# Optimization experiments

Hardware: AMD Instinct MI355X
Metric: run time of the kernel (lower is better)

Reference implementation:

```python
import jax, jax.numpy as jnp
import numpy as np

HID, INNER, CONV, L, DR = 1024, 2048, 4, 16, 64
B, S = 1, 2048


def setup_inputs() -> dict:
    key = jax.random.key(0)
    ks = jax.random.split(key, 8)
    def n(k, shape, scale=0.02):
        return jax.random.normal(k, shape, jnp.float32) * scale
    x = jax.random.normal(ks[0], (B, S, HID), jnp.float32)
    W_in = n(ks[1], (HID, 2 * INNER))                 # input_proj kernel (no bias)
    conv_w = n(ks[2], (CONV, 1, INNER), 0.1)          # depthwise conv kernel (W, I/g, O)
    conv_b = n(ks[3], (INNER,), 0.01)                 # conv bias
    W_x = n(ks[4], (INNER, DR + 2 * L))               # x_proj kernel (no bias)
    W_delta = n(ks[5], (DR, INNER), 0.05)             # delta_proj kernel
    b_delta = jnp.zeros((INNER,), jnp.float32)        # delta_proj bias
    A_log = jnp.log(jnp.tile(jnp.arange(1, L + 1, dtype=jnp.float32), (INNER, 1)))
    D = jnp.ones((INNER,), jnp.float32)
    W_out = n(ks[6], (INNER, HID))                    # out_proj kernel (no bias)
    return dict(x=x, W_in=W_in, conv_w=conv_w, conv_b=conv_b, W_x=W_x,
                W_delta=W_delta, b_delta=b_delta, A_log=A_log, D=D, W_out=W_out)


def _combine(left, right):
    # Associative op for linear recurrence h_t = a_t * h_{t-1} + b_t
    a1, b1 = left
    a2, b2 = right
    return a1 * a2, a2 * b1 + b2


def reference(x, W_in, conv_w, conv_b, W_x, W_delta, b_delta, A_log, D, W_out):
    b, s, _ = x.shape
    xz = x @ W_in                                     # [b,s,2*INNER]
    xi, z = xz[..., :INNER], xz[..., INNER:]
    # depthwise causal-ish conv: pad conv_dim-1 both sides (flax int padding), keep first s
    xc = jax.lax.conv_general_dilated(
        xi, conv_w, window_strides=(1,), padding=[(CONV - 1, CONV - 1)],
        dimension_numbers=('NWC', 'WIO', 'NWC'), feature_group_count=INNER)
    xc = jax.nn.silu(xc[:, :s, :] + conv_b)           # [b,s,INNER]
    # selective SSM
    A = -jnp.exp(A_log.astype(jnp.float32))           # [INNER,L]
    Df = D.astype(jnp.float32)
    xp = xc @ W_x                                     # [b,s,DR+2L]
    delta, Bm, Cm = xp[..., :DR], xp[..., DR:DR + L], xp[..., DR + L:]
    delta = jax.nn.softplus(delta @ W_delta + b_delta)  # [b,s,INNER]
    deltaA = jnp.exp(jnp.einsum('bsd,dl->bsdl', delta, A))            # [b,s,d,l]
    deltaBx = jnp.einsum('bsd,bsl,bsd->bsdl', delta, Bm, xc)          # [b,s,d,l]
    _, h = jax.lax.associative_scan(_combine, (deltaA, deltaBx), axis=1)
    y = jnp.einsum('bsdl,bsl->bsd', h, Cm) + xc * Df  # [b,s,INNER]
    y = y * jax.nn.silu(z)
    return y @ W_out                                  # [b,s,HID]
```

## Files before the change

kernel.cpp:

```cpp
#include <hip/hip_runtime.h>
#include <hip/hip_bf16.h>
#include <math.h>

#define S_LEN 2048
#define HID   1024
#define INNER 2048
#define NCONV 4
#define LSTATE 16
#define DRANK 64
#define XPW   96
#define CHUNK 32
#define NCHUNK (S_LEN / CHUNK)
#define XPAD  128
#define XPSPLIT 16
#define OSPLIT  4

typedef __attribute__((ext_vector_type(8))) short bf16x8;
typedef __attribute__((ext_vector_type(4))) float f32x4;

__device__ __forceinline__ short f2bf(float f) {
  union { __hip_bfloat16 h; short s; } u;
  u.h = __float2bfloat16(f);
  return u.s;
}

__device__ __forceinline__ float fexp(float x) { return __expf(x); }

#define GLDS(gp, lp) __builtin_amdgcn_global_load_lds(                         \
    (const __attribute__((address_space(1))) unsigned int*)(gp),               \
    (__attribute__((address_space(3))) unsigned int*)(lp), 16, 0, 0)

#define NB_CAST (S_LEN * HID / 4 / 256)
#define NB_WIN  ((2 * INNER / 32) * (HID / 32))
#define NB_WOUT ((HID / 32) * (INNER / 32))
#define NB_WX   ((XPAD / 32) * (INNER / 32))
#define NB_WD   ((INNER / 32) * (DRANK / 32))
#define NB_PREP (NB_CAST + NB_WIN + NB_WOUT + NB_WX + NB_WD)
__global__ __launch_bounds__(256) void prep_kernel(
    const float* __restrict__ x, short* __restrict__ xb,
    const float* __restrict__ W_in, short* __restrict__ WinT,
    const float* __restrict__ W_out, short* __restrict__ WoutT,
    const float* __restrict__ W_x, short* __restrict__ WxT,
    const float* __restrict__ W_delta, short* __restrict__ WdT) {
  const int b = blockIdx.x;
  if (b < NB_CAST) {
    int i = b * 256 + threadIdx.x;
    const float4 v = ((const float4*)x)[i];
    short4 o;
    o.x = f2bf(v.x); o.y = f2bf(v.y); o.z = f2bf(v.z); o.w = f2bf(v.w);
    ((short4*)xb)[i] = o;
    return;
  }
  __shared__ float tile[32][33];
  const float* in; short* outp; int R, C, bx, by;
  if (b < NB_CAST + NB_WIN) {
    int bb = b - NB_CAST;
    in = W_in; outp = WinT; R = HID; C = 2 * INNER;
    bx = bb % (2 * INNER / 32); by = bb / (2 * INNER / 32);
  } else if (b < NB_CAST + NB_WIN + NB_WOUT) {
    int bb = b - NB_CAST - NB_WIN;
    in = W_out; outp = WoutT; R = INNER; C = HID;
    bx = bb % (HID / 32); by = bb / (HID / 32);
  } else if (b < NB_CAST + NB_WIN + NB_WOUT + NB_WX) {
    int bb = b - NB_CAST - NB_WIN - NB_WOUT;
    in = W_x; outp = WxT; R = INNER; C = XPW;
    bx = bb % (XPAD / 32); by = bb / (XPAD / 32);
  } else {
    int bb = b - NB_CAST - NB_WIN - NB_WOUT - NB_WX;
    in = W_delta; outp = WdT; R = DRANK; C = INNER;
    bx = bb % (INNER / 32); by = bb / (INNER / 32);
  }
  const int bc = bx * 32, br = by * 32;
  const int tx = threadIdx.x & 31, ty = threadIdx.x >> 5;
  #pragma unroll
  for (int i = 0; i < 32; i += 8)
    tile[ty + i][tx] = (bc + tx < C)
        ? in[(size_t)(br + ty + i) * C + bc + tx] : 0.f;
  __syncthreads();
  #pragma unroll
  for (int i = 0; i < 32; i += 8)
    outp[(size_t)(bc + ty + i) * R + br + tx] = f2bf(tile[tx][ty + i]);
}

#define BK   32
#define NBUF 4
template<int EPI>
__global__ __launch_bounds__(512) void gemm_bf16(
    const short* __restrict__ A,  int lda,
    const short* __restrict__ Bt, int ldb,
    float* __restrict__ C, int ldc,
    int kPerSplit, size_t cSliceStride,
    const float* __restrict__ bias) {
  __shared__ short As[NBUF][128 * BK];
  __shared__ short Bs[NBUF][128 * BK];
  const int tid  = threadIdx.x;
  const int lane = tid & 63;
  const int wave = tid >> 6;
  const int bm = blockIdx.y * 128;
  const int bn = blockIdx.x * 128;
  const int wm = (wave & 1) * 64;
  const int wn = (wave >> 1) * 32;
  const int fr = lane & 15;
  const int fq = lane >> 4;
  const int kbeg = blockIdx.z * kPerSplit;
  const int nIter = kPerSplit / BK;
  float* Cw = C + (size_t)blockIdx.z * cSliceStride;

  const int sw  = wave & 3;
  const int rs0 = sw * 32 + (lane >> 2);
  const int rs1 = rs0 + 16;
  const int sg0 = (lane & 3) ^ ((rs0 >> 1) & 3);
  const int sg1 = (lane & 3) ^ ((rs1 >> 1) & 3);
  const bool isB = wave >= 4;
  const short* gbase = isB ? Bt : A;
  const int    gld   = isB ? ldb : lda;
  const int    gro   = isB ? bn  : bm;
  const short* g0 = gbase + (size_t)(gro + rs0) * gld + kbeg + sg0 * 8;
  const short* g1 = gbase + (size_t)(gro + rs1) * gld + kbeg + sg1 * 8;
  const int lo0 = (sw * 32) * BK;
  const int lo1 = (sw * 32 + 16) * BK;

  f32x4 acc[4][2] = {};

#define STAGE(tile, buf) do {                                                  \
    short* dst_ = isB ? &Bs[buf][0] : &As[buf][0];                             \
    const int ko_ = (tile) * BK;                                               \
    GLDS(g0 + ko_, dst_ + lo0);                                                \
    GLDS(g1 + ko_, dst_ + lo1);                                                \
  } while (0)

  STAGE(0, 0);
  if (nIter > 1) STAGE(1, 1);
  if (nIter > 2) STAGE(2, 2);

  const int sl = (fq ^ ((fr >> 1) & 3)) * 8;
  for (int t = 0; t < nIter; ++t) {
    const int rem = nIter - 1 - t;
    if (rem >= 2)      asm volatile("s_waitcnt vmcnt(4)" ::: "memory");
    else if (rem == 1) asm volatile("s_waitcnt vmcnt(2)" ::: "memory");
    else               asm volatile("s_waitcnt vmcnt(0)" ::: "memory");
    asm volatile("s_barrier" ::: "memory");
    if (t + 3 < nIter) STAGE(t + 3, (t + 3) & 3);
    const int r = t & 3;
    bf16x8 af[4], bfv[2];
    #pragma unroll
    for (int mi = 0; mi < 4; ++mi)
      af[mi] = *(const bf16x8*)(&As[r][(wm + mi * 16 + fr) * BK + sl]);
    #pragma unroll
    for (int ni = 0; ni < 2; ++ni)
      bfv[ni] = *(const bf16x8*)(&Bs[r][(wn + ni * 16 + fr) * BK + sl]);
    #pragma unroll
    for (int mi = 0; mi < 4; ++mi)
      #pragma unroll
      for (int ni = 0; ni < 2; ++ni)
        acc[mi][ni] = __builtin_amdgcn_mfma_f32_16x16x32_bf16(
            af[mi], bfv[ni], acc[mi][ni], 0, 0, 0);
  }
#undef STAGE
  #pragma unroll
  for (int mi = 0; mi < 4; ++mi) {
    #pragma unroll
    for (int ni = 0; ni < 2; ++ni) {
      const int col = bn + wn + ni * 16 + fr;
      #pragma unroll
      for (int r = 0; r < 4; ++r) {
        const int row = bm + wm + mi * 16 + fq * 4 + r;
        float v = acc[mi][ni][r];
        if (EPI == 1) {
          v += bias[col];
          v = fmaxf(v, 0.f) + log1pf(expf(-fabsf(v)));
        }
        Cw[(size_t)row * ldc + col] = v;
      }
    }
  }
}

__global__ __launch_bounds__(256) void reduce_xp_kernel(
    const float* __restrict__ part, float* __restrict__ xp,
    short* __restrict__ xpb64) {
  int i4 = blockIdx.x * 256 + threadIdx.x;
  if (i4 >= S_LEN * (XPW / 4)) return;
  int m = i4 / (XPW / 4);
  int n4 = i4 - m * (XPW / 4);
  const float4* p = (const float4*)part;
  const size_t rowv = (size_t)m * (XPAD / 4) + n4;
  const size_t slice = (size_t)S_LEN * (XPAD / 4);
  float4 o = p[rowv];
  #pragma unroll
  for (int s = 1; s < XPSPLIT; ++s) {
    float4 v = p[rowv + s * slice];
    o.x += v.x; o.y += v.y; o.z += v.z; o.w += v.w;
  }
  ((float4*)xp)[i4] = o;
  if (n4 < DRANK / 4) {
    short4 s4;
    s4.x = f2bf(o.x); s4.y = f2bf(o.y); s4.z = f2bf(o.z); s4.w = f2bf(o.w);
    ((short4*)xpb64)[m * (DRANK / 4) + n4] = s4;
  }
}

__global__ __launch_bounds__(256) void reduce_out_kernel(
    const float* __restrict__ part, float* __restrict__ out) {
  int i4 = blockIdx.x * 256 + threadIdx.x;
  if (i4 >= S_LEN * (HID / 4)) return;
  const float4* p = (const float4*)part;
  const size_t slice = (size_t)S_LEN * (HID / 4);
  float4 o = p[i4];
  #pragma unroll
  for (int s = 1; s < OSPLIT; ++s) {
    float4 v = p[i4 + s * slice];
    o.x += v.x; o.y += v.y; o.z += v.z; o.w += v.w;
  }
  ((float4*)out)[i4] = o;
}

__global__ __launch_bounds__(256) void conv_silu_kernel(
    const float* __restrict__ xz,
    const float* __restrict__ cw,
    const float* __restrict__ cb,
    float* __restrict__ xc,
    short* __restrict__ xcb) {
  int i4 = blockIdx.x * 256 + threadIdx.x;
  if (i4 >= S_LEN * INNER / 4) return;
  int s = i4 / (INNER / 4);
  int cg = i4 - s * (INNER / 4);
  float4 acc = ((const float4*)cb)[cg];
  #pragma unroll
  for (int k = 0; k < NCONV; ++k) {
    int t = s - (NCONV - 1) + k;
    if (t >= 0) {
      float4 xv = *(const float4*)(xz + (size_t)t * (2 * INNER) + cg * 4);
      float4 wv = ((const float4*)(cw + k * INNER))[cg];
      acc.x += xv.x * wv.x; acc.y += xv.y * wv.y;
      acc.z += xv.z * wv.z; acc.w += xv.w * wv.w;
    }
  }
  float4 v;
  v.x = acc.x / (1.f + fexp(-acc.x));
  v.y = acc.y / (1.f + fexp(-acc.y));
  v.z = acc.z / (1.f + fexp(-acc.z));
  v.w = acc.w / (1.f + fexp(-acc.w));
  ((float4*)xc)[i4] = v;
  short4 o;
  o.x = f2bf(v.x); o.y = f2bf(v.y); o.z = f2bf(v.z); o.w = f2bf(v.w);
  ((short4*)xcb)[i4] = o;
}


__global__ __launch_bounds__(256) void scan_pass1(
    const float* __restrict__ delta,
    const float* __restrict__ xp,
    const float* __restrict__ xc,
    const float* __restrict__ A_log,
    float* __restrict__ Aprod,
    float* __restrict__ Hend) {
  __shared__ float Bc[CHUNK][LSTATE];
  const int tid = threadIdx.x;
  const int d = blockIdx.y * 256 + tid;
  const int c = blockIdx.x;
  const int s0 = c * CHUNK;
  for (int u = tid; u < CHUNK * LSTATE; u += 256) {
    int r = u >> 4, l = u & 15;
    Bc[r][l] = xp[(size_t)(s0 + r) * XPW + DRANK + l];
  }
  float a[LSTATE];
  {
    const float4* Ar = (const float4*)(A_log + (size_t)d * LSTATE);
    #pragma unroll
    for (int q = 0; q < 4; ++q) {
      float4 v = Ar[q];
      a[q * 4 + 0] = -fexp(v.x);
      a[q * 4 + 1] = -fexp(v.y);
      a[q * 4 + 2] = -fexp(v.z);
      a[q * 4 + 3] = -fexp(v.w);
    }
  }
  float h[LSTATE] = {}, ap[LSTATE];
  #pragma unroll
  for (int l = 0; l < LSTATE; ++l) ap[l] = 1.f;
  __syncthreads();
  const float* pd = delta + (size_t)s0 * INNER + d;
  const float* px = xc    + (size_t)s0 * INNER + d;
  for (int i = 0; i < CHUNK; ++i) {
    float dv = *pd, xcv = *px;
    pd += INNER; px += INNER;
    float sc = dv * xcv;
    #pragma unroll
    for (int l = 0; l < LSTATE; ++l) {
      float dA = fexp(dv * a[l]);
      h[l] = fmaf(dA, h[l], sc * Bc[i][l]);
      ap[l] *= dA;
    }
  }
  float4* Ap = (float4*)(Aprod + ((size_t)c * INNER + d) * LSTATE);
  float4* Hp = (float4*)(Hend  + ((size_t)c * INNER + d) * LSTATE);
  #pragma unroll
  for (int q = 0; q < 4; ++q) {
    Ap[q] = make_float4(ap[q * 4], ap[q * 4 + 1], ap[q * 4 + 2], ap[q * 4 + 3]);
    Hp[q] = make_float4(h[q * 4], h[q * 4 + 1], h[q * 4 + 2], h[q * 4 + 3]);
  }
}

__global__ __launch_bounds__(256) void scan_pass2(
    const float* __restrict__ Aprod, const float* __restrict__ Hend,
    float* __restrict__ Hin) {
  const int idx = blockIdx.x * 256 + threadIdx.x;
  const size_t stride = (size_t)INNER * LSTATE;
  float h = 0.f;
  for (int cb = 0; cb < NCHUNK; cb += 16) {
    float ap[16], he[16];
    #pragma unroll
    for (int j = 0; j < 16; ++j) {
      size_t o = (size_t)(cb + j) * stride + idx;
      ap[j] = Aprod[o];
      he[j] = Hend[o];
    }
    #pragma unroll
    for (int j = 0; j < 16; ++j) {
      size_t o = (size_t)(cb + j) * stride + idx;
      Hin[o] = h;
      h = ap[j] * h + he[j];
    }
  }
}

__global__ __launch_bounds__(256) void scan_pass3(
    const float* __restrict__ delta,
    const float* __restrict__ xp,
    const float* __restrict__ xc,
    const float* __restrict__ xz,
    const float* __restrict__ A_log,
    const float* __restrict__ Dvec,
    const float* __restrict__ Hin,
    short* __restrict__ ybf) {
  __shared__ float Bc[CHUNK][LSTATE];
  __shared__ float Cc[CHUNK][LSTATE];
  const int tid = threadIdx.x;
  const int d = blockIdx.y * 256 + tid;
  const int c = blockIdx.x;
  const int s0 = c * CHUNK;
  for (int u = tid; u < CHUNK * LSTATE; u += 256) {
    int r = u >> 4, l = u & 15;
    size_t base = (size_t)(s0 + r) * XPW + DRANK;
    Bc[r][l] = xp[base + l];
    Cc[r][l] = xp[base + LSTATE + l];
  }
  float a[LSTATE], h[LSTATE];
  {
    const float4* Ar = (const float4*)(A_log + (size_t)d * LSTATE);
    #pragma unroll
    for (int q = 0; q < 4; ++q) {
      float4 v = Ar[q];
      a[q * 4 + 0] = -fexp(v.x);
      a[q * 4 + 1] = -fexp(v.y);
      a[q * 4 + 2] = -fexp(v.z);
      a[q * 4 + 3] = -fexp(v.w);
    }
    const float4* Hi = (const float4*)(Hin + ((size_t)c * INNER + d) * LSTATE);
    #pragma unroll
    for (int q = 0; q < 4; ++q) {
      float4 v = Hi[q];
      h[q * 4 + 0] = v.x; h[q * 4 + 1] = v.y;
      h[q * 4 + 2] = v.z; h[q * 4 + 3] = v.w;
    }
  }
  const float Dd = Dvec[d];
  __syncthreads();
  const float* pd = delta + (size_t)s0 * INNER + d;
  const float* px = xc    + (size_t)s0 * INNER + d;
  const float* pz = xz + (size_t)s0 * (2 * INNER) + INNER + d;
  short* py = ybf + (size_t)s0 * INNER + d;
  for (int i = 0; i < CHUNK; ++i) {
    float dv = *pd, xcv = *px, zv = *pz;
    pd += INNER; px += INNER; pz += 2 * INNER;
    float sc = dv * xcv;
    float contrib = 0.f;
    #pragma unroll
    for (int l = 0; l < LSTATE; ++l) {
      float dA = fexp(dv * a[l]);
      h[l] = fmaf(dA, h[l], sc * Bc[i][l]);
      contrib = fmaf(h[l], Cc[i][l], contrib);
    }
    float silu_z = zv / (1.f + fexp(-zv));
    *py = f2bf(fmaf(xcv, Dd, contrib) * silu_z);
    py += INNER;
  }
}

extern "C" void kernel_launch(void* const* d_in, const int* in_sizes, int n_in,
                              void* d_out, int out_size, void* d_ws, size_t ws_size,
                              hipStream_t stream) {
  const float* x      = (const float*)d_in[0];
  const float* W_in   = (const float*)d_in[1];
  const float* conv_w = (const float*)d_in[2];
  const float* conv_b = (const float*)d_in[3];
  const float* W_x    = (const float*)d_in[4];
  const float* W_delta= (const float*)d_in[5];
  const float* b_delta= (const float*)d_in[6];
  const float* A_log  = (const float*)d_in[7];
  const float* Dvec   = (const float*)d_in[8];
  const float* W_out  = (const float*)d_in[9];
  float* out = (float*)d_out;

  float* ws    = (float*)d_ws;
  float* xz    = ws;
  float* xc    = xz + (size_t)S_LEN * 2 * INNER;
  float* xp    = xc + (size_t)S_LEN * INNER;
  float* delta = xp + (size_t)S_LEN * XPW;
  float* Aprod = delta + (size_t)S_LEN * INNER;
  float* Hend  = Aprod + (size_t)NCHUNK * INNER * LSTATE;
  float* Hin   = Hend  + (size_t)NCHUNK * INNER * LSTATE;
  short* xb    = (short*)(Hin + (size_t)NCHUNK * INNER * LSTATE);
  short* WinT  = xb + (size_t)S_LEN * HID;
  short* WoutT = WinT + (size_t)(2 * INNER) * HID;
  short* ybf   = WoutT + (size_t)HID * INNER;
  short* xcb   = ybf + (size_t)S_LEN * INNER;
  short* WxT   = xcb + (size_t)S_LEN * INNER;
  short* WdT   = WxT + (size_t)XPAD * INNER;
  short* xpb64 = WdT + (size_t)INNER * DRANK;
  float* xpPart  = Aprod;
  float* outPart = xc;

  prep_kernel<<<NB_PREP, 256, 0, stream>>>(
      x, xb, W_in, WinT, W_out, WoutT, W_x, WxT, W_delta, WdT);

  gemm_bf16<0><<<dim3(4096 / 128, 2048 / 128, 1), 512, 0, stream>>>(
      xb, HID, WinT, HID, xz, 2 * INNER, HID, 0, nullptr);

  conv_silu_kernel<<<(S_LEN * INNER / 4 + 255) / 256, 256, 0, stream>>>(
      xz, conv_w, conv_b, xc, xcb);

  gemm_bf16<0><<<dim3(1, 2048 / 128, XPSPLIT), 512, 0, stream>>>(
      xcb, INNER, WxT, INNER, xpPart, XPAD, INNER / XPSPLIT,
      (size_t)S_LEN * XPAD, nullptr);
  reduce_xp_kernel<<<(S_LEN * (XPW / 4) + 255) / 256, 256, 0, stream>>>(
      xpPart, xp, xpb64);

  gemm_bf16<1><<<dim3(2048 / 128, 2048 / 128, 1), 512, 0, stream>>>(
      xpb64, DRANK, WdT, DRANK, delta, INNER, DRANK, 0, b_delta);

  scan_pass1<<<dim3(NCHUNK, INNER / 256), 256, 0, stream>>>(
      delta, xp, xc, A_log, Aprod, Hend);
  scan_pass2<<<(INNER * LSTATE) / 256, 256, 0, stream>>>(Aprod, Hend, Hin);
  scan_pass3<<<dim3(NCHUNK, INNER / 256), 256, 0, stream>>>(
      delta, xp, xc, xz, A_log, Dvec, Hin, ybf);

  gemm_bf16<0><<<dim3(1024 / 128, 2048 / 128, OSPLIT), 512, 0, stream>>>(
      ybf, INNER, WoutT, INNER, outPart, HID, INNER / OSPLIT,
      (size_t)S_LEN * HID, nullptr);
  reduce_out_kernel<<<(S_LEN * (HID / 4) + 255) / 256, 256, 0, stream>>>(
      outPart, out);
}
```

Baseline: 169.8 us.

## Fuse three scan passes into one cooperative kernel with grid syncs

Merges the chunk-local scan, the cross-chunk prefix pass and the output pass into a single cooperatively launched kernel that uses grid-wide barriers in place of separate launches. This removes two kernel launches and keeps the A/B/C chunk data in shared memory across phases, so it is not reloaded. The grid of 64x8=512 blocks of 256 threads must all be co-resident for the cooperative launch to work, and grid syncs add their own cost. It also halves the output GEMM split-K factor (OSPLIT 4->2).

```diff
diff --git a/kernel.cpp b/kernel.cpp
--- a/kernel.cpp
+++ b/kernel.cpp
@@ -1,6 +1,9 @@
 #include <hip/hip_runtime.h>
 #include <hip/hip_bf16.h>
+#include <hip/hip_cooperative_groups.h>
 #include <math.h>
+
+namespace cg = cooperative_groups;
 
 #define S_LEN 2048
 #define HID   1024
@@ -13,7 +16,7 @@
 #define NCHUNK (S_LEN / CHUNK)
 #define XPAD  128
 #define XPSPLIT 16
-#define OSPLIT  4
+#define OSPLIT  2
 
 typedef __attribute__((ext_vector_type(8))) short bf16x8;
 typedef __attribute__((ext_vector_type(4))) float f32x4;
@@ -247,92 +250,16 @@
   ((short4*)xcb)[i4] = o;
 }
 
-
-__global__ __launch_bounds__(256) void scan_pass1(
-    const float* __restrict__ delta,
-    const float* __restrict__ xp,
-    const float* __restrict__ xc,
-    const float* __restrict__ A_log,
-    float* __restrict__ Aprod,
-    float* __restrict__ Hend) {
-  __shared__ float Bc[CHUNK][LSTATE];
-  const int tid = threadIdx.x;
-  const int d = blockIdx.y * 256 + tid;
-  const int c = blockIdx.x;
-  const int s0 = c * CHUNK;
-  for (int u = tid; u < CHUNK * LSTATE; u += 256) {
-    int r = u >> 4, l = u & 15;
-    Bc[r][l] = xp[(size_t)(s0 + r) * XPW + DRANK + l];
-  }
-  float a[LSTATE];
-  {
-    const float4* Ar = (const float4*)(A_log + (size_t)d * LSTATE);
-    #pragma unroll
-    for (int q = 0; q < 4; ++q) {
-      float4 v = Ar[q];
-      a[q * 4 + 0] = -fexp(v.x);
-      a[q * 4 + 1] = -fexp(v.y);
-      a[q * 4 + 2] = -fexp(v.z);
-      a[q * 4 + 3] = -fexp(v.w);
-    }
-  }
-  float h[LSTATE] = {}, ap[LSTATE];
-  #pragma unroll
-  for (int l = 0; l < LSTATE; ++l) ap[l] = 1.f;
-  __syncthreads();
-  const float* pd = delta + (size_t)s0 * INNER + d;
-  const float* px = xc    + (size_t)s0 * INNER + d;
-  for (int i = 0; i < CHUNK; ++i) {
-    float dv = *pd, xcv = *px;
-    pd += INNER; px += INNER;
-    float sc = dv * xcv;
-    #pragma unroll
-    for (int l = 0; l < LSTATE; ++l) {
-      float dA = fexp(dv * a[l]);
-      h[l] = fmaf(dA, h[l], sc * Bc[i][l]);
-      ap[l] *= dA;
-    }
-  }
-  float4* Ap = (float4*)(Aprod + ((size_t)c * INNER + d) * LSTATE);
-  float4* Hp = (float4*)(Hend  + ((size_t)c * INNER + d) * LSTATE);
-  #pragma unroll
-  for (int q = 0; q < 4; ++q) {
-    Ap[q] = make_float4(ap[q * 4], ap[q * 4 + 1], ap[q * 4 + 2], ap[q * 4 + 3]);
-    Hp[q] = make_float4(h[q * 4], h[q * 4 + 1], h[q * 4 + 2], h[q * 4 + 3]);
-  }
-}
-
-__global__ __launch_bounds__(256) void scan_pass2(
-    const float* __restrict__ Aprod, const float* __restrict__ Hend,
-    float* __restrict__ Hin) {
-  const int idx = blockIdx.x * 256 + threadIdx.x;
-  const size_t stride = (size_t)INNER * LSTATE;
-  float h = 0.f;
-  for (int cb = 0; cb < NCHUNK; cb += 16) {
-    float ap[16], he[16];
-    #pragma unroll
-    for (int j = 0; j < 16; ++j) {
-      size_t o = (size_t)(cb + j) * stride + idx;
-      ap[j] = Aprod[o];
-      he[j] = Hend[o];
-    }
-    #pragma unroll
-    for (int j = 0; j < 16; ++j) {
-      size_t o = (size_t)(cb + j) * stride + idx;
-      Hin[o] = h;
-      h = ap[j] * h + he[j];
-    }
-  }
-}
-
-__global__ __launch_bounds__(256) void scan_pass3(
+__global__ __launch_bounds__(256) void scan_fused(
     const float* __restrict__ delta,
     const float* __restrict__ xp,
     const float* __restrict__ xc,
     const float* __restrict__ xz,
     const float* __restrict__ A_log,
     const float* __restrict__ Dvec,
-    const float* __restrict__ Hin,
+    float* __restrict__ Aprod,
+    float* __restrict__ Hend,
+    float* __restrict__ Hin,
     short* __restrict__ ybf) {
   __shared__ float Bc[CHUNK][LSTATE];
   __shared__ float Cc[CHUNK][LSTATE];
@@ -346,7 +273,7 @@
     Bc[r][l] = xp[base + l];
     Cc[r][l] = xp[base + LSTATE + l];
   }
-  float a[LSTATE], h[LSTATE];
+  float a[LSTATE];
   {
     const float4* Ar = (const float4*)(A_log + (size_t)d * LSTATE);
     #pragma unroll
@@ -357,6 +284,60 @@
       a[q * 4 + 2] = -fexp(v.z);
       a[q * 4 + 3] = -fexp(v.w);
     }
+  }
+  __syncthreads();
+  {
+    float h[LSTATE] = {}, ap[LSTATE];
+    #pragma unroll
+    for (int l = 0; l < LSTATE; ++l) ap[l] = 1.f;
+    const float* pd = delta + (size_t)s0 * INNER + d;
+    const float* px = xc    + (size_t)s0 * INNER + d;
+    for (int i = 0; i < CHUNK; ++i) {
+      float dv = *pd, xcv = *px;
+      pd += INNER; px += INNER;
+      float sc = dv * xcv;
+      #pragma unroll
+      for (int l = 0; l < LSTATE; ++l) {
+        float dA = fexp(dv * a[l]);
+        h[l] = fmaf(dA, h[l], sc * Bc[i][l]);
+        ap[l] *= dA;
+      }
+    }
+    float4* Ap = (float4*)(Aprod + ((size_t)c * INNER + d) * LSTATE);
+    float4* Hp = (float4*)(Hend  + ((size_t)c * INNER + d) * LSTATE);
+    #pragma unroll
+    for (int q = 0; q < 4; ++q) {
+      Ap[q] = make_float4(ap[q * 4], ap[q * 4 + 1], ap[q * 4 + 2], ap[q * 4 + 3]);
+      Hp[q] = make_float4(h[q * 4], h[q * 4 + 1], h[q * 4 + 2], h[q * 4 + 3]);
+    }
+  }
+  cg::this_grid().sync();
+  {
+    const int flat = blockIdx.y * NCHUNK + blockIdx.x;
+    if (flat < (INNER * LSTATE) / 256) {
+      const int idx = flat * 256 + tid;
+      const size_t stride = (size_t)INNER * LSTATE;
+      float h = 0.f;
+      for (int cb = 0; cb < NCHUNK; cb += 16) {
+        float ap[16], he[16];
+        #pragma unroll
+        for (int j = 0; j < 16; ++j) {
+          size_t o = (size_t)(cb + j) * stride + idx;
+          ap[j] = Aprod[o];
+          he[j] = Hend[o];
+        }
+        #pragma unroll
+        for (int j = 0; j < 16; ++j) {
+          size_t o = (size_t)(cb + j) * stride + idx;
+          Hin[o] = h;
+          h = ap[j] * h + he[j];
+        }
+      }
+    }
+  }
+  cg::this_grid().sync();
+  {
+    float h[LSTATE];
     const float4* Hi = (const float4*)(Hin + ((size_t)c * INNER + d) * LSTATE);
     #pragma unroll
     for (int q = 0; q < 4; ++q) {
@@ -364,27 +345,26 @@
       h[q * 4 + 0] = v.x; h[q * 4 + 1] = v.y;
       h[q * 4 + 2] = v.z; h[q * 4 + 3] = v.w;
     }
-  }
-  const float Dd = Dvec[d];
-  __syncthreads();
-  const float* pd = delta + (size_t)s0 * INNER + d;
-  const float* px = xc    + (size_t)s0 * INNER + d;
-  const float* pz = xz + (size_t)s0 * (2 * INNER) + INNER + d;
-  short* py = ybf + (size_t)s0 * INNER + d;
-  for (int i = 0; i < CHUNK; ++i) {
-    float dv = *pd, xcv = *px, zv = *pz;
-    pd += INNER; px += INNER; pz += 2 * INNER;
-    float sc = dv * xcv;
-    float contrib = 0.f;
-    #pragma unroll
-    for (int l = 0; l < LSTATE; ++l) {
-      float dA = fexp(dv * a[l]);
-      h[l] = fmaf(dA, h[l], sc * Bc[i][l]);
-      contrib = fmaf(h[l], Cc[i][l], contrib);
-    }
-    float silu_z = zv / (1.f + fexp(-zv));
-    *py = f2bf(fmaf(xcv, Dd, contrib) * silu_z);
-    py += INNER;
+    const float Dd = Dvec[d];
+    const float* pd = delta + (size_t)s0 * INNER + d;
+    const float* px = xc    + (size_t)s0 * INNER + d;
+    const float* pz = xz + (size_t)s0 * (2 * INNER) + INNER + d;
+    short* py = ybf + (size_t)s0 * INNER + d;
+    for (int i = 0; i < CHUNK; ++i) {
+      float dv = *pd, xcv = *px, zv = *pz;
+      pd += INNER; px += INNER; pz += 2 * INNER;
+      float sc = dv * xcv;
+      float contrib = 0.f;
+      #pragma unroll
+      for (int l = 0; l < LSTATE; ++l) {
+        float dA = fexp(dv * a[l]);
+        h[l] = fmaf(dA, h[l], sc * Bc[i][l]);
+        contrib = fmaf(h[l], Cc[i][l], contrib);
+      }
+      float silu_z = zv / (1.f + fexp(-zv));
+      *py = f2bf(fmaf(xcv, Dd, contrib) * silu_z);
+      py += INNER;
+    }
   }
 }
 
@@ -440,11 +420,14 @@
   gemm_bf16<1><<<dim3(2048 / 128, 2048 / 128, 1), 512, 0, stream>>>(
       xpb64, DRANK, WdT, DRANK, delta, INNER, DRANK, 0, b_delta);
 
-  scan_pass1<<<dim3(NCHUNK, INNER / 256), 256, 0, stream>>>(
-      delta, xp, xc, A_log, Aprod, Hend);
-  scan_pass2<<<(INNER * LSTATE) / 256, 256, 0, stream>>>(Aprod, Hend, Hin);
-  scan_pass3<<<dim3(NCHUNK, INNER / 256), 256, 0, stream>>>(
-      delta, xp, xc, xz, A_log, Dvec, Hin, ybf);
+  {
+    void* args[] = {(void*)&delta, (void*)&xp, (void*)&xc, (void*)&xz,
+                    (void*)&A_log, (void*)&Dvec, (void*)&Aprod, (void*)&Hend,
+                    (void*)&Hin, (void*)&ybf};
+    hipLaunchCooperativeKernel((const void*)scan_fused,
+                               dim3(NCHUNK, INNER / 256), dim3(256),
+                               args, 0, stream);
+  }
 
   gemm_bf16<0><<<dim3(1024 / 128, 2048 / 128, OSPLIT), 512, 0, stream>>>(
       ybf, INNER, WoutT, INNER, outPart, HID, INNER / OSPLIT,
```

Measured after the change: 306.1 us. +80.3%, slower.
